# Kernel optimization log

Hardware: AMD Instinct MI355X
Metric: run time of the kernel (lower is better)

Reference implementation:

```python
import jax, jax.numpy as jnp
import numpy as np
from jax import lax

IN_CH = 256
OUT_CH = 256
INTER = IN_CH // 2
KERNEL = 3


def setup_inputs() -> dict:
    key = jax.random.key(0)
    ks = jax.random.split(key, 6)
    B, C, H, W = 8, IN_CH, 128, 128
    x = jax.random.normal(ks[0], (B, C, H, W), dtype=jnp.float32)
    s = 1.0 / np.sqrt(C)
    Wq = jax.random.normal(ks[1], (INTER, C), dtype=jnp.float32) * s
    Wk = jax.random.normal(ks[2], (INTER, C), dtype=jnp.float32) * s
    Wv = jax.random.normal(ks[3], (INTER, C), dtype=jnp.float32) * s
    w1d = jax.random.normal(ks[4], (KERNEL,), dtype=jnp.float32) * (1.0 / np.sqrt(KERNEL))
    Wc = jax.random.normal(ks[5], (OUT_CH, INTER, 3, 3), dtype=jnp.float32) * (1.0 / np.sqrt(INTER * 9))
    return {"x": x, "Wq": Wq, "Wk": Wk, "Wv": Wv, "w1d": w1d, "Wc": Wc}


def reference(x, Wq, Wk, Wv, w1d, Wc):
    B, C, H, W = x.shape
    inter = Wq.shape[0]
    Hs, Ws = H // 4, W // 4  # 1x1 conv, stride 4, pad 0 == spatial subsample
    xs = x[:, :, ::4, ::4]  # [B, C, Hs, Ws]
    q = jnp.einsum('oc,bchw->bohw', Wq, xs).reshape(B, inter, Hs * Ws)  # [B, inter, N]
    k = jnp.einsum('oc,bchw->bohw', Wk, xs).reshape(B, inter, Hs * Ws)
    v = jnp.einsum('oc,bchw->bohw', Wv, xs).reshape(B, inter, Hs * Ws)
    # gate = softmax(Q^T K) over last dim, shape [B, N, N]
    scores = jnp.einsum('bcn,bcm->bnm', q, k)
    gate = jax.nn.softmax(scores, axis=-1)
    # gated value: [B, inter, N] -> [B, inter, Hs, Ws]
    gv = jnp.einsum('bnm,bcm->bcn', gate, v).reshape(B, inter, Hs, Ws)
    # ECA channel gating: global avg pool -> conv1d over channel dim -> sigmoid
    ca = gv.mean(axis=(2, 3))  # [B, inter]
    ca = lax.conv_general_dilated(
        ca[:, None, :],                     # [B, 1, inter]
        w1d[None, None, :],                 # [1, 1, K]
        window_strides=(1,), padding=[((KERNEL - 1) // 2,) * 2],
        dimension_numbers=('NCH', 'OIH', 'NCH'))
    ca = jax.nn.sigmoid(ca)[:, 0, :, None, None]  # [B, inter, 1, 1]
    out = gv * ca
    out = lax.conv_general_dilated(
        out, Wc, window_strides=(1, 1), padding='SAME',
        dimension_numbers=('NCHW', 'OIHW', 'NCHW'))
    return out, gate, ca
```

## Files before the change

### kernel.cpp

```cpp
#include <hip/hip_runtime.h>
#include <math.h>

#define B_   8
#define C_   256
#define CI_  128
#define N_   1024
#define HW_  32
#define CO_  256

typedef __bf16 v8bf __attribute__((ext_vector_type(8)));
typedef float  f32x4 __attribute__((ext_vector_type(4)));
typedef unsigned short ushort_t;

__device__ __forceinline__ unsigned short f2bf_rne(float f) {
    unsigned int u = __float_as_uint(f);
    unsigned int r = u + 0x7FFF + ((u >> 16) & 1);
    return (unsigned short)(r >> 16);
}
__device__ __forceinline__ float bf2f(unsigned short h) {
    return __uint_as_float(((unsigned int)h) << 16);
}
__device__ __forceinline__ v8bf ld8(const ushort_t* p) {
    return *(const v8bf*)p;
}

__global__ __launch_bounds__(256) void prep_all_kernel(
    const float* __restrict__ Wc,
    const float* __restrict__ Wq, const float* __restrict__ Wk,
    const float* __restrict__ Wv,
    ushort_t* __restrict__ Whi, ushort_t* __restrict__ Wlo,
    ushort_t* __restrict__ Wp_hi, ushort_t* __restrict__ Wp_lo,
    float* __restrict__ meanb)
{
    const int bx = blockIdx.x;
    const int tid = threadIdx.x;

    if (bx < 1152) {
        if (bx == 0) {
            *(float4*)&meanb[tid * 4] = make_float4(0.f, 0.f, 0.f, 0.f);
        }
        int idx = bx * 256 + tid;
        int o = idx / 1152;
        int r = idx - o * 1152;
        int ci = r / 9;
        int tap = r - ci * 9;
        float v = Wc[idx];
        unsigned short h = f2bf_rne(v);
        unsigned short l = f2bf_rne(v - bf2f(h));
        int didx = o * 1152 + tap * 128 + ci;
        Whi[didx] = h; Wlo[didx] = l;
    } else {
        int j = (bx - 1152) * 256 + tid;
        int o = j >> 8, c = j & 255;
        float v = (o < 128) ? Wq[o * 256 + c]
                : (o < 256) ? Wk[(o - 128) * 256 + c]
                            : Wv[(o - 256) * 256 + c];
        unsigned short h = f2bf_rne(v);
        unsigned short l = f2bf_rne(v - bf2f(h));
        Wp_hi[j] = h; Wp_lo[j] = l;
    }
}

__global__ __launch_bounds__(256) void proj_fused_kernel(
    const float* __restrict__ x,
    const ushort_t* __restrict__ Wp_hi, const ushort_t* __restrict__ Wp_lo,
    ushort_t* __restrict__ qt_hi, ushort_t* __restrict__ qt_lo,
    ushort_t* __restrict__ kt_hi, ushort_t* __restrict__ kt_lo,
    ushort_t* __restrict__ vB_hi, ushort_t* __restrict__ vB_lo)
{
    __shared__ __align__(16) char xsm[32768];
    const int lin = blockIdx.x;
    const int b  = lin & 7;
    const int n5 = lin >> 3;
    const int n0 = n5 * 32;
    const int tid = threadIdx.x;

    {
        const int w = tid & 31, cg = tid >> 5;
        #pragma unroll
        for (int j = 0; j < 4; ++j) {
            const int cbase = j * 64 + cg * 8;
            float v[8];
            #pragma unroll
            for (int i = 0; i < 8; ++i)
                v[i] = x[((size_t)(b * C_ + cbase + i) * 128 + n5 * 4) * 128 + w * 4];
            unsigned int hw[4], lw[4];
            #pragma unroll
            for (int p = 0; p < 4; ++p) {
                unsigned short h0 = f2bf_rne(v[2 * p]);
                unsigned short l0 = f2bf_rne(v[2 * p] - bf2f(h0));
                unsigned short h1 = f2bf_rne(v[2 * p + 1]);
                unsigned short l1 = f2bf_rne(v[2 * p + 1] - bf2f(h1));
                hw[p] = (unsigned)h0 | ((unsigned)h1 << 16);
                lw[p] = (unsigned)l0 | ((unsigned)l1 << 16);
            }
            const int chunk = j * 8 + cg;
            const int addr = w * 512 + ((chunk ^ (w & 7)) << 4);
            *(uint4*)&xsm[addr]         = make_uint4(hw[0], hw[1], hw[2], hw[3]);
            *(uint4*)&xsm[16384 + addr] = make_uint4(lw[0], lw[1], lw[2], lw[3]);
        }
    }
    __syncthreads();

    const int l = tid & 63, wv = tid >> 6;
    const int ln = l & 15, quad = l >> 4;

    f32x4 acc[6][2];
    #pragma unroll
    for (int t = 0; t < 6; ++t)
        #pragma unroll
        for (int j = 0; j < 2; ++j) acc[t][j] = (f32x4){0.f,0.f,0.f,0.f};

    #pragma unroll 2
    for (int k0 = 0; k0 < 256; k0 += 32) {
        v8bf Bh[2], Bl[2];
        #pragma unroll
        for (int j = 0; j < 2; ++j) {
            int row = j * 16 + ln;
            int chunk = (k0 >> 3) + quad;
            int addr = row * 512 + ((chunk ^ (row & 7)) << 4);
            Bh[j] = *(const v8bf*)&xsm[addr];
            Bl[j] = *(const v8bf*)&xsm[16384 + addr];
        }
        v8bf Ah[6], Al[6];
        #pragma unroll
        for (int t = 0; t < 6; ++t) {
            int st = wv + 4 * t;
            size_t off = (size_t)(st * 16 + ln) * 256 + k0 + quad * 8;
            Ah[t] = ld8(Wp_hi + off); Al[t] = ld8(Wp_lo + off);
        }
        __builtin_amdgcn_s_setprio(1);
        #pragma unroll
        for (int t = 0; t < 4; ++t)
            #pragma unroll
            for (int j = 0; j < 2; ++j) {
                acc[t][j] = __builtin_amdgcn_mfma_f32_16x16x32_bf16(Ah[t], Bh[j], acc[t][j], 0, 0, 0);
                acc[t][j] = __builtin_amdgcn_mfma_f32_16x16x32_bf16(Ah[t], Bl[j], acc[t][j], 0, 0, 0);
                acc[t][j] = __builtin_amdgcn_mfma_f32_16x16x32_bf16(Al[t], Bh[j], acc[t][j], 0, 0, 0);
            }
        #pragma unroll
        for (int t = 4; t < 6; ++t)
            #pragma unroll
            for (int j = 0; j < 2; ++j) {
                acc[t][j] = __builtin_amdgcn_mfma_f32_16x16x32_bf16(Bh[j], Ah[t], acc[t][j], 0, 0, 0);
                acc[t][j] = __builtin_amdgcn_mfma_f32_16x16x32_bf16(Bh[j], Al[t], acc[t][j], 0, 0, 0);
                acc[t][j] = __builtin_amdgcn_mfma_f32_16x16x32_bf16(Bl[j], Ah[t], acc[t][j], 0, 0, 0);
            }
        __builtin_amdgcn_s_setprio(0);
    }

    #pragma unroll
    for (int t = 0; t < 4; ++t) {
        const int st = wv + 4 * t;
        ushort_t* th = (t < 2) ? qt_hi : kt_hi;
        ushort_t* tl = (t < 2) ? qt_lo : kt_lo;
        const int oo = (st & 7) * 16 + quad * 4;
        #pragma unroll
        for (int j = 0; j < 2; ++j) {
            int n = n0 + j * 16 + ln;
            unsigned int h01 = 0, h23 = 0, l01 = 0, l23 = 0;
            #pragma unroll
            for (int r = 0; r < 4; ++r) {
                float f = acc[t][j][r];
                unsigned short hh = f2bf_rne(f);
                unsigned short lo = f2bf_rne(f - bf2f(hh));
                if (r < 2) { h01 |= ((unsigned)hh) << (16 * r); l01 |= ((unsigned)lo) << (16 * r); }
                else       { h23 |= ((unsigned)hh) << (16 * (r - 2)); l23 |= ((unsigned)lo) << (16 * (r - 2)); }
            }
            size_t off = ((size_t)(b * N_) + n) * 128 + oo;
            *(uint2*)&th[off] = make_uint2(h01, h23);
            *(uint2*)&tl[off] = make_uint2(l01, l23);
        }
    }
    #pragma unroll
    for (int t = 4; t < 6; ++t) {
        const int st = wv + 4 * t;
        const int c = (st - 16) * 16 + ln;
        #pragma unroll
        for (int j = 0; j < 2; ++j) {
            int mlo = j * 16 + quad * 4;
            unsigned int h01 = 0, h23 = 0, l01 = 0, l23 = 0;
            #pragma unroll
            for (int r = 0; r < 4; ++r) {
                float f = acc[t][j][r];
                unsigned short hh = f2bf_rne(f);
                unsigned short lo = f2bf_rne(f - bf2f(hh));
                if (r < 2) { h01 |= ((unsigned)hh) << (16 * r); l01 |= ((unsigned)lo) << (16 * r); }
                else       { h23 |= ((unsigned)hh) << (16 * (r - 2)); l23 |= ((unsigned)lo) << (16 * (r - 2)); }
            }
            size_t off = (((size_t)b * 32 + n5) * 128 + c) * 32 + mlo;
            *(uint2*)&vB_hi[off] = make_uint2(h01, h23);
            *(uint2*)&vB_lo[off] = make_uint2(l01, l23);
        }
    }
}

__global__ __launch_bounds__(512, 2) void attn_fused_kernel(
    const ushort_t* __restrict__ qt_hi, const ushort_t* __restrict__ qt_lo,
    const ushort_t* __restrict__ kt_hi, const ushort_t* __restrict__ kt_lo,
    const ushort_t* __restrict__ vB_hi, const ushort_t* __restrict__ vB_lo,
    float* __restrict__ gate, float* __restrict__ gv, float* __restrict__ meanb)
{
    __shared__ __align__(16) char gsm[65536];
    __shared__ float redA[8][32];
    __shared__ float redB[8][32];

    const int lin = blockIdx.x + 32 * blockIdx.y;
    const int b  = lin & 7;
    const int n0 = (lin >> 3) * 32;
    const int tid = threadIdx.x;
    const int l = tid & 63, w = tid >> 6;
    const int ln = l & 15, quad = l >> 4;
    const int Mw = w * 128;

    const ushort_t* qb_h = qt_hi + ((size_t)(b * N_) + n0) * 128;
    const ushort_t* qb_l = qt_lo + ((size_t)(b * N_) + n0) * 128;
    const ushort_t* kb_h = kt_hi + (size_t)(b * N_) * 128;
    const ushort_t* kb_l = kt_lo + (size_t)(b * N_) * 128;

    f32x4 acc[2][8];
    #pragma unroll
    for (int nt = 0; nt < 2; ++nt)
        #pragma unroll
        for (int mt = 0; mt < 8; ++mt) acc[nt][mt] = (f32x4){0.f,0.f,0.f,0.f};

    #pragma unroll
    for (int c0 = 0; c0 < 128; c0 += 32) {
        v8bf Ah[2], Al[2];
        #pragma unroll
        for (int nt = 0; nt < 2; ++nt) {
            size_t aoff = (size_t)(nt * 16 + ln) * 128 + c0 + quad * 8;
            Ah[nt] = ld8(qb_h + aoff); Al[nt] = ld8(qb_l + aoff);
        }
        #pragma unroll
        for (int mt = 0; mt < 8; ++mt) {
            size_t boff = (size_t)(Mw + mt * 16 + ln) * 128 + c0 + quad * 8;
            v8bf Bh = ld8(kb_h + boff);
            v8bf Bl = ld8(kb_l + boff);
            __builtin_amdgcn_s_setprio(1);
            #pragma unroll
            for (int nt = 0; nt < 2; ++nt) {
                acc[nt][mt] = __builtin_amdgcn_mfma_f32_16x16x32_bf16(Ah[nt], Bh, acc[nt][mt], 0, 0, 0);
                acc[nt][mt] = __builtin_amdgcn_mfma_f32_16x16x32_bf16(Ah[nt], Bl, acc[nt][mt], 0, 0, 0);
                acc[nt][mt] = __builtin_amdgcn_mfma_f32_16x16x32_bf16(Al[nt], Bh, acc[nt][mt], 0, 0, 0);
            }
            __builtin_amdgcn_s_setprio(0);
        }
    }

    float rmax[2][4];
    #pragma unroll
    for (int nt = 0; nt < 2; ++nt)
        #pragma unroll
        for (int r = 0; r < 4; ++r) {
            float m = acc[nt][0][r];
            #pragma unroll
            for (int mt = 1; mt < 8; ++mt) m = fmaxf(m, acc[nt][mt][r]);
            rmax[nt][r] = m;
        }
    #pragma unroll
    for (int nt = 0; nt < 2; ++nt)
        #pragma unroll
        for (int r = 0; r < 4; ++r) {
            float m = rmax[nt][r];
            #pragma unroll
            for (int xm = 1; xm <= 8; xm <<= 1) m = fmaxf(m, __shfl_xor(m, xm, 64));
            rmax[nt][r] = m;
        }
    if (ln == 0) {
        #pragma unroll
        for (int nt = 0; nt < 2; ++nt)
            #pragma unroll
            for (int r = 0; r < 4; ++r)
                redA[w][nt * 16 + quad * 4 + r] = rmax[nt][r];
    }
    __syncthreads();
    #pragma unroll
    for (int nt = 0; nt < 2; ++nt)
        #pragma unroll
        for (int r = 0; r < 4; ++r) {
            int row = nt * 16 + quad * 4 + r;
            float m0 = fmaxf(fmaxf(redA[0][row], redA[1][row]),
                             fmaxf(redA[2][row], redA[3][row]));
            float m1 = fmaxf(fmaxf(redA[4][row], redA[5][row]),
                             fmaxf(redA[6][row], redA[7][row]));
            rmax[nt][r] = fmaxf(m0, m1);
        }

    float rsum[2][4];
    #pragma unroll
    for (int nt = 0; nt < 2; ++nt)
        #pragma unroll
        for (int r = 0; r < 4; ++r) {
            float s = 0.f;
            #pragma unroll
            for (int mt = 0; mt < 8; ++mt) {
                float e = __expf(acc[nt][mt][r] - rmax[nt][r]);
                acc[nt][mt][r] = e;
                s += e;
            }
            rsum[nt][r] = s;
        }
    #pragma unroll
    for (int nt = 0; nt < 2; ++nt)
        #pragma unroll
        for (int r = 0; r < 4; ++r) {
            float s = rsum[nt][r];
            #pragma unroll
            for (int xm = 1; xm <= 8; xm <<= 1) s += __shfl_xor(s, xm, 64);
            rsum[nt][r] = s;
        }
    if (ln == 0) {
        #pragma unroll
        for (int nt = 0; nt < 2; ++nt)
            #pragma unroll
            for (int r = 0; r < 4; ++r)
                redB[w][nt * 16 + quad * 4 + r] = rsum[nt][r];
    }
    __syncthreads();
    #pragma unroll
    for (int nt = 0; nt < 2; ++nt)
        #pragma unroll
        for (int r = 0; r < 4; ++r) {
            int row = nt * 16 + quad * 4 + r;
            float inv = 1.0f / ((redB[0][row] + redB[1][row] + redB[2][row] + redB[3][row]) +
                                (redB[4][row] + redB[5][row] + redB[6][row] + redB[7][row]));
            #pragma unroll
            for (int mt = 0; mt < 8; ++mt) acc[nt][mt][r] *= inv;
        }

    #pragma unroll
    for (int nt = 0; nt < 2; ++nt)
        #pragma unroll
        for (int r = 0; r < 4; ++r) {
            int nl = nt * 16 + quad * 4 + r;
            #pragma unroll
            for (int mt = 0; mt < 8; ++mt) {
                int m = Mw + mt * 16 + ln;
                int chunk = m >> 3;
                int addr = nl * 2048 + (((chunk ^ (nl & 7))) << 4) + ((m & 7) << 1);
                *(ushort_t*)&gsm[addr] = f2bf_rne(acc[nt][mt][r]);
            }
        }
    __syncthreads();

    const ushort_t* vb_h = vB_hi + (size_t)b * CI_ * N_;
    const ushort_t* vb_l = vB_lo + (size_t)b * CI_ * N_;

    f32x4 acc2[2];
    acc2[0] = (f32x4){0.f,0.f,0.f,0.f};
    acc2[1] = (f32x4){0.f,0.f,0.f,0.f};

    #pragma unroll 4
    for (int m0 = 0; m0 < 1024; m0 += 32) {
        v8bf Bg[2];
        #pragma unroll
        for (int nt = 0; nt < 2; ++nt) {
            int nl = nt * 16 + ln;
            int chunk = (m0 >> 3) + quad;
            Bg[nt] = *(const v8bf*)&gsm[nl * 2048 + (((chunk ^ (nl & 7))) << 4)];
        }
        int c = w * 16 + ln;
        size_t aoff = (((size_t)(m0 >> 5)) * 128 + c) * 32 + quad * 8;
        v8bf Avh = ld8(vb_h + aoff);
        v8bf Avl = ld8(vb_l + aoff);
        __builtin_amdgcn_s_setprio(1);
        #pragma unroll
        for (int nt = 0; nt < 2; ++nt) {
            acc2[nt] = __builtin_amdgcn_mfma_f32_16x16x32_bf16(Avh, Bg[nt], acc2[nt], 0, 0, 0);
            acc2[nt] = __builtin_amdgcn_mfma_f32_16x16x32_bf16(Avl, Bg[nt], acc2[nt], 0, 0, 0);
        }
        __builtin_amdgcn_s_setprio(0);
    }

    #pragma unroll
    for (int nt = 0; nt < 2; ++nt) {
        int n = n0 + nt * 16 + ln;
        float4 o4 = make_float4(acc2[nt][0], acc2[nt][1], acc2[nt][2], acc2[nt][3]);
        *(float4*)&gv[((size_t)(b * N_) + n) * CI_ + w * 16 + quad * 4] = o4;
    }

    float* grow = gate + (size_t)b * N_ * N_;
    #pragma unroll
    for (int nt = 0; nt < 2; ++nt)
        #pragma unroll
        for (int r = 0; r < 4; ++r) {
            int n = n0 + nt * 16 + quad * 4 + r;
            #pragma unroll
            for (int mt = 0; mt < 8; ++mt) {
                int m = Mw + mt * 16 + ln;
                grow[(size_t)n * N_ + m] = acc[nt][mt][r];
            }
        }

    float s0 = acc2[0][0] + acc2[1][0];
    float s1 = acc2[0][1] + acc2[1][1];
    float s2 = acc2[0][2] + acc2[1][2];
    float s3 = acc2[0][3] + acc2[1][3];
    #pragma unroll
    for (int xm = 1; xm <= 8; xm <<= 1) {
        s0 += __shfl_xor(s0, xm, 64);
        s1 += __shfl_xor(s1, xm, 64);
        s2 += __shfl_xor(s2, xm, 64);
        s3 += __shfl_xor(s3, xm, 64);
    }
    if (ln == 0) {
        int cb = b * CI_ + w * 16 + quad * 4;
        atomicAdd(&meanb[cb + 0], s0);
        atomicAdd(&meanb[cb + 1], s1);
        atomicAdd(&meanb[cb + 2], s2);
        atomicAdd(&meanb[cb + 3], s3);
    }
}

__global__ __launch_bounds__(256) void gvca_prep_kernel(
    const float* __restrict__ gv, const float* __restrict__ meanb,
    const float* __restrict__ w1d,
    ushort_t* __restrict__ gvh, ushort_t* __restrict__ gvl,
    float* __restrict__ ca_out)
{
    __shared__ float ca_s[128];
    const int lin = blockIdx.x;
    const int b  = lin & 7;
    const int ns = lin >> 3;
    const int tid = threadIdx.x;

    if (tid < 128) {
        const float sc = 1.0f / 1024.0f;
        int t = b * 128 + tid;
        float left  = (tid > 0)   ? meanb[t - 1] * sc : 0.0f;
        float mid   = meanb[t] * sc;
        float right = (tid < 127) ? meanb[t + 1] * sc : 0.0f;
        float val = w1d[0] * left + w1d[1] * mid + w1d[2] * right;
        float s = 1.0f / (1.0f + __expf(-val));
        ca_s[tid] = s;
        if (ns == 0) ca_out[t] = s;
    }
    __syncthreads();

    const int cl = (tid & 31) * 4;
    const int nr = tid >> 5;
    #pragma unroll
    for (int i = 0; i < 4; ++i) {
        int n = ns * 32 + nr + i * 8;
        size_t off = ((size_t)(b * N_) + n) * 128 + cl;
        float4 v4 = *(const float4*)&gv[off];
        float vv[4] = { v4.x * ca_s[cl], v4.y * ca_s[cl + 1],
                        v4.z * ca_s[cl + 2], v4.w * ca_s[cl + 3] };
        unsigned int h01 = 0, h23 = 0, l01 = 0, l23 = 0;
        #pragma unroll
        for (int t = 0; t < 4; ++t) {
            unsigned short h = f2bf_rne(vv[t]);
            unsigned short lo = f2bf_rne(vv[t] - bf2f(h));
            if (t < 2) { h01 |= ((unsigned)h) << (16 * t); l01 |= ((unsigned)lo) << (16 * t); }
            else       { h23 |= ((unsigned)h) << (16 * (t - 2)); l23 |= ((unsigned)lo) << (16 * (t - 2)); }
        }
        *(uint2*)&gvh[off] = make_uint2(h01, h23);
        *(uint2*)&gvl[off] = make_uint2(l01, l23);
    }
}

#define CV_BHI  0
#define CV_BLO  26112
__global__ __launch_bounds__(512, 1) void conv_mfma_kernel(
    const ushort_t* __restrict__ gvh, const ushort_t* __restrict__ gvl,
    const ushort_t* __restrict__ Whi, const ushort_t* __restrict__ Wlo,
    float* __restrict__ out)
{
    extern __shared__ __align__(16) char smem[];
    const int AH[2] = {52224, 68608};
    const int AL[2] = {60416, 76800};

    const int lin = blockIdx.x;
    const int b    = lin & 7;
    const int rest = lin >> 3;
    const int o0 = (rest & 3) * 64;
    const int h0 = (rest >> 2) * 4;
    const int tid = threadIdx.x;
    const int l   = tid & 63;
    const int wv  = tid >> 6;
    const int wy  = wv >> 2;
    const int wx  = wv & 3;
    const int ln  = l & 15;
    const int quad = l >> 4;

    f32x4 acc[2][2];
    #pragma unroll
    for (int i = 0; i < 2; ++i)
        #pragma unroll
        for (int j = 0; j < 2; ++j)
            acc[i][j] = (f32x4){0.f, 0.f, 0.f, 0.f};

    const int srow = tid >> 3, scol = tid & 7;
    const int la   = srow * 128 + scol * 16;
    const int csrc = scol ^ (srow & 7);

    for (int half = 0; half < 2; ++half) {
        __syncthreads();
        for (int u = tid; u < 204 * 8; u += 512) {
            int p  = u >> 3;
            int cs = u & 7;
            int hrel = p / 34;
            int c    = p - hrel * 34;
            int gr = h0 + hrel - 1;
            int gc = c - 1;
            bool ok = ((unsigned)gr < 32u) && ((unsigned)gc < 32u);
            uint4 h4 = make_uint4(0, 0, 0, 0), l4 = make_uint4(0, 0, 0, 0);
            if (ok) {
                size_t src = ((size_t)(b * N_) + gr * 32 + gc) * 128 + half * 64 + cs * 8;
                h4 = *(const uint4*)&gvh[src];
                l4 = *(const uint4*)&gvl[src];
            }
            int addr = p * 128 + ((cs ^ (p & 7)) << 4);
            *(uint4*)&smem[CV_BHI + addr] = h4;
            *(uint4*)&smem[CV_BLO + addr] = l4;
        }
        {
            size_t g = (size_t)(o0 + srow) * 1152 + half * 64 + csrc * 8;
            *(uint4*)&smem[AH[0] + la] = *(const uint4*)&Whi[g];
            *(uint4*)&smem[AL[0] + la] = *(const uint4*)&Wlo[g];
        }

        for (int tap = 0; tap < 9; ++tap) {
            __syncthreads();
            uint4 nh, nl;
            if (tap < 8) {
                size_t g = (size_t)(o0 + srow) * 1152 + (tap + 1) * 128 + half * 64 + csrc * 8;
                nh = *(const uint4*)&Whi[g];
                nl = *(const uint4*)&Wlo[g];
            }
            const int ah = AH[tap & 1], al = AL[tap & 1];
            const int dy = tap / 3, dx = tap - dy * 3;
            const int pbase = (wx + dy) * 34 + dx;
            #pragma unroll
            for (int cc = 0; cc < 2; ++cc) {
                v8bf Bh[2], Bl[2], Ah2[2], Al2[2];
                #pragma unroll
                for (int j = 0; j < 2; ++j) {
                    int p = pbase + j * 16 + ln;
                    int ch = cc * 4 + quad;
                    int addr = p * 128 + ((ch ^ (p & 7)) << 4);
                    Bh[j] = *(const v8bf*)&smem[CV_BHI + addr];
                    Bl[j] = *(const v8bf*)&smem[CV_BLO + addr];
                }
                #pragma unroll
                for (int i = 0; i < 2; ++i) {
                    int o = wy * 32 + i * 16 + ln;
                    int ch = cc * 4 + quad;
                    int addr = o * 128 + ((ch ^ (o & 7)) << 4);
                    Ah2[i] = *(const v8bf*)&smem[ah + addr];
                    Al2[i] = *(const v8bf*)&smem[al + addr];
                }
                __builtin_amdgcn_s_setprio(1);
                #pragma unroll
                for (int i = 0; i < 2; ++i)
                    #pragma unroll
                    for (int j = 0; j < 2; ++j) {
                        acc[i][j] = __builtin_amdgcn_mfma_f32_16x16x32_bf16(Ah2[i], Bh[j], acc[i][j], 0, 0, 0);
                        acc[i][j] = __builtin_amdgcn_mfma_f32_16x16x32_bf16(Ah2[i], Bl[j], acc[i][j], 0, 0, 0);
                        acc[i][j] = __builtin_amdgcn_mfma_f32_16x16x32_bf16(Al2[i], Bh[j], acc[i][j], 0, 0, 0);
                    }
                __builtin_amdgcn_s_setprio(0);
            }
            if (tap < 8) {
                int nb = (tap + 1) & 1;
                *(uint4*)&smem[AH[nb] + la] = nh;
                *(uint4*)&smem[AL[nb] + la] = nl;
            }
        }
    }

    const int h = h0 + wx;
    #pragma unroll
    for (int i = 0; i < 2; ++i)
        #pragma unroll
        for (int j = 0; j < 2; ++j)
            #pragma unroll
            for (int r = 0; r < 4; ++r) {
                int o = o0 + wy * 32 + i * 16 + quad * 4 + r;
                int w = j * 16 + ln;
                out[(size_t)(b * CO_ + o) * N_ + h * 32 + w] = acc[i][j][r];
            }
}

extern "C" void kernel_launch(void* const* d_in, const int* in_sizes, int n_in,
                              void* d_out, int out_size, void* d_ws, size_t ws_size,
                              hipStream_t stream) {
    const float* x   = (const float*)d_in[0];
    const float* Wq  = (const float*)d_in[1];
    const float* Wk  = (const float*)d_in[2];
    const float* Wv  = (const float*)d_in[3];
    const float* w1d = (const float*)d_in[4];
    const float* Wc  = (const float*)d_in[5];

    float* out  = (float*)d_out;
    float* gate = out + 2097152;
    float* ca   = gate + 8388608;

    float*    gv      = (float*)d_ws;
    float*    meanb   = gv + 1048576;
    ushort_t* Whi     = (ushort_t*)(meanb + 1024);
    ushort_t* Wlo     = Whi + 294912;
    ushort_t* Wp_hi   = Wlo + 294912;
    ushort_t* Wp_lo   = Wp_hi + 98304;
    ushort_t* qt_hi   = Wp_lo + 98304;
    ushort_t* qt_lo   = qt_hi + 1048576;
    ushort_t* kt_hi   = qt_lo + 1048576;
    ushort_t* kt_lo   = kt_hi + 1048576;
    ushort_t* vB_hi   = kt_lo + 1048576;
    ushort_t* vB_lo   = vB_hi + 1048576;
    ushort_t* gvh     = vB_lo + 1048576;
    ushort_t* gvl     = gvh + 1048576;

    static bool s_attr_done = false;
    if (!s_attr_done) {
        hipFuncSetAttribute((const void*)conv_mfma_kernel,
                            hipFuncAttributeMaxDynamicSharedMemorySize, 84992);
        s_attr_done = true;
    }

    prep_all_kernel<<<dim3(1536), 256, 0, stream>>>(
        Wc, Wq, Wk, Wv, Whi, Wlo, Wp_hi, Wp_lo, meanb);
    proj_fused_kernel<<<dim3(256), 256, 0, stream>>>(
        x, Wp_hi, Wp_lo, qt_hi, qt_lo, kt_hi, kt_lo, vB_hi, vB_lo);
    attn_fused_kernel<<<dim3(32, 8), 512, 0, stream>>>(
        qt_hi, qt_lo, kt_hi, kt_lo, vB_hi, vB_lo, gate, gv, meanb);
    gvca_prep_kernel<<<dim3(256), 256, 0, stream>>>(
        gv, meanb, w1d, gvh, gvl, ca);
    conv_mfma_kernel<<<dim3(256), 512, 84992, stream>>>(
        gvh, gvl, Whi, Wlo, out);
}
```

Measured before the change: 265.1 us.

## Fuse channel-attention gating into attention kernel via cooperative grid sync

Merges the ECA gating/bf16-split pass into the attention kernel. A cooperative launch with a grid-wide barrier waits until all channel-mean atomics have landed, then each block scales its register-resident gv tile and writes the hi/lo bf16 split directly. This removes one kernel launch and the fp32 gv round trip through global memory. In exchange, the grid barrier requires all 256 blocks to be co-resident and adds a global synchronization stall.

```diff
diff --git a/kernel.cpp b/kernel.cpp
--- a/kernel.cpp
+++ b/kernel.cpp
@@ -1,4 +1,5 @@
 #include <hip/hip_runtime.h>
+#include <hip/hip_cooperative_groups.h>
 #include <math.h>
 
 #define B_   8
@@ -199,11 +200,15 @@
     const ushort_t* __restrict__ qt_hi, const ushort_t* __restrict__ qt_lo,
     const ushort_t* __restrict__ kt_hi, const ushort_t* __restrict__ kt_lo,
     const ushort_t* __restrict__ vB_hi, const ushort_t* __restrict__ vB_lo,
-    float* __restrict__ gate, float* __restrict__ gv, float* __restrict__ meanb)
+    float* __restrict__ gate, float* __restrict__ meanb,
+    const float* __restrict__ w1d,
+    ushort_t* __restrict__ gvh, ushort_t* __restrict__ gvl,
+    float* __restrict__ ca_out)
 {
     __shared__ __align__(16) char gsm[65536];
     __shared__ float redA[8][32];
     __shared__ float redB[8][32];
+    __shared__ float ca_s[128];
 
     const int lin = blockIdx.x + 32 * blockIdx.y;
     const int b  = lin & 7;
@@ -373,13 +378,6 @@
         __builtin_amdgcn_s_setprio(0);
     }
 
-    #pragma unroll
-    for (int nt = 0; nt < 2; ++nt) {
-        int n = n0 + nt * 16 + ln;
-        float4 o4 = make_float4(acc2[nt][0], acc2[nt][1], acc2[nt][2], acc2[nt][3]);
-        *(float4*)&gv[((size_t)(b * N_) + n) * CI_ + w * 16 + quad * 4] = o4;
-    }
-
     float* grow = gate + (size_t)b * N_ * N_;
     #pragma unroll
     for (int nt = 0; nt < 2; ++nt)
@@ -411,19 +409,9 @@
         atomicAdd(&meanb[cb + 2], s2);
         atomicAdd(&meanb[cb + 3], s3);
     }
-}
-
-__global__ __launch_bounds__(256) void gvca_prep_kernel(
-    const float* __restrict__ gv, const float* __restrict__ meanb,
-    const float* __restrict__ w1d,
-    ushort_t* __restrict__ gvh, ushort_t* __restrict__ gvl,
-    float* __restrict__ ca_out)
-{
-    __shared__ float ca_s[128];
-    const int lin = blockIdx.x;
-    const int b  = lin & 7;
-    const int ns = lin >> 3;
-    const int tid = threadIdx.x;
+
+    __threadfence();
+    cooperative_groups::this_grid().sync();
 
     if (tid < 128) {
         const float sc = 1.0f / 1024.0f;
@@ -434,27 +422,26 @@
         float val = w1d[0] * left + w1d[1] * mid + w1d[2] * right;
         float s = 1.0f / (1.0f + __expf(-val));
         ca_s[tid] = s;
-        if (ns == 0) ca_out[t] = s;
+        if (n0 == 0) ca_out[t] = s;
     }
     __syncthreads();
 
-    const int cl = (tid & 31) * 4;
-    const int nr = tid >> 5;
-    #pragma unroll
-    for (int i = 0; i < 4; ++i) {
-        int n = ns * 32 + nr + i * 8;
-        size_t off = ((size_t)(b * N_) + n) * 128 + cl;
-        float4 v4 = *(const float4*)&gv[off];
-        float vv[4] = { v4.x * ca_s[cl], v4.y * ca_s[cl + 1],
-                        v4.z * ca_s[cl + 2], v4.w * ca_s[cl + 3] };
+    #pragma unroll
+    for (int nt = 0; nt < 2; ++nt) {
+        int n  = n0 + nt * 16 + ln;
+        int c0 = w * 16 + quad * 4;
+        float vv[4];
+        #pragma unroll
+        for (int r = 0; r < 4; ++r) vv[r] = acc2[nt][r] * ca_s[c0 + r];
         unsigned int h01 = 0, h23 = 0, l01 = 0, l23 = 0;
         #pragma unroll
-        for (int t = 0; t < 4; ++t) {
-            unsigned short h = f2bf_rne(vv[t]);
-            unsigned short lo = f2bf_rne(vv[t] - bf2f(h));
-            if (t < 2) { h01 |= ((unsigned)h) << (16 * t); l01 |= ((unsigned)lo) << (16 * t); }
-            else       { h23 |= ((unsigned)h) << (16 * (t - 2)); l23 |= ((unsigned)lo) << (16 * (t - 2)); }
-        }
+        for (int r = 0; r < 4; ++r) {
+            unsigned short h = f2bf_rne(vv[r]);
+            unsigned short lo = f2bf_rne(vv[r] - bf2f(h));
+            if (r < 2) { h01 |= ((unsigned)h) << (16 * r); l01 |= ((unsigned)lo) << (16 * r); }
+            else       { h23 |= ((unsigned)h) << (16 * (r - 2)); l23 |= ((unsigned)lo) << (16 * (r - 2)); }
+        }
+        size_t off = ((size_t)(b * N_) + n) * 128 + c0;
         *(uint2*)&gvh[off] = make_uint2(h01, h23);
         *(uint2*)&gvl[off] = make_uint2(l01, l23);
     }
@@ -597,8 +584,7 @@
     float* gate = out + 2097152;
     float* ca   = gate + 8388608;
 
-    float*    gv      = (float*)d_ws;
-    float*    meanb   = gv + 1048576;
+    float*    meanb   = (float*)d_ws;
     ushort_t* Whi     = (ushort_t*)(meanb + 1024);
     ushort_t* Wlo     = Whi + 294912;
     ushort_t* Wp_hi   = Wlo + 294912;
@@ -623,10 +609,15 @@
         Wc, Wq, Wk, Wv, Whi, Wlo, Wp_hi, Wp_lo, meanb);
     proj_fused_kernel<<<dim3(256), 256, 0, stream>>>(
         x, Wp_hi, Wp_lo, qt_hi, qt_lo, kt_hi, kt_lo, vB_hi, vB_lo);
-    attn_fused_kernel<<<dim3(32, 8), 512, 0, stream>>>(
-        qt_hi, qt_lo, kt_hi, kt_lo, vB_hi, vB_lo, gate, gv, meanb);
-    gvca_prep_kernel<<<dim3(256), 256, 0, stream>>>(
-        gv, meanb, w1d, gvh, gvl, ca);
+
+    void* attn_args[] = {
+        (void*)&qt_hi, (void*)&qt_lo, (void*)&kt_hi, (void*)&kt_lo,
+        (void*)&vB_hi, (void*)&vB_lo, (void*)&gate, (void*)&meanb,
+        (void*)&w1d, (void*)&gvh, (void*)&gvl, (void*)&ca
+    };
+    hipLaunchCooperativeKernel((void*)attn_fused_kernel, dim3(32, 8), dim3(512),
+                               attn_args, 0, stream);
+
     conv_mfma_kernel<<<dim3(256), 512, 84992, stream>>>(
         gvh, gvl, Whi, Wlo, out);
 }
```

After: 379.4 us. +43.1%, slower.

## Halve attention row tile to 16 rows and stage gate writes through LDS

Applied to the files above, without the earlier changes.

Each attention block now handles 16 query rows instead of 32, which doubles the grid to 512 blocks and halves LDS and accumulator registers so more blocks fit per CU. The gate matrix is no longer written straight from MFMA fragments, which gave scattered 4-byte stores. It is now staged through shared memory in two 8-row passes and written out as coalesced float4 rows. The trade-off is that K and V loads from global memory are repeated across twice as many blocks, and the extra synchronisation passes add overhead.

```diff
diff --git a/kernel.cpp b/kernel.cpp
--- a/kernel.cpp
+++ b/kernel.cpp
@@ -195,19 +195,19 @@
     }
 }
 
-__global__ __launch_bounds__(512, 2) void attn_fused_kernel(
+__global__ __launch_bounds__(512, 4) void attn_fused_kernel(
     const ushort_t* __restrict__ qt_hi, const ushort_t* __restrict__ qt_lo,
     const ushort_t* __restrict__ kt_hi, const ushort_t* __restrict__ kt_lo,
     const ushort_t* __restrict__ vB_hi, const ushort_t* __restrict__ vB_lo,
     float* __restrict__ gate, float* __restrict__ gv, float* __restrict__ meanb)
 {
-    __shared__ __align__(16) char gsm[65536];
-    __shared__ float redA[8][32];
-    __shared__ float redB[8][32];
-
-    const int lin = blockIdx.x + 32 * blockIdx.y;
+    __shared__ __align__(16) char gsm[32768];
+    __shared__ float redA[8][16];
+    __shared__ float redB[8][16];
+
+    const int lin = blockIdx.x;
     const int b  = lin & 7;
-    const int n0 = (lin >> 3) * 32;
+    const int n0 = (lin >> 3) * 16;
     const int tid = threadIdx.x;
     const int l = tid & 63, w = tid >> 6;
     const int ln = l & 15, quad = l >> 4;
@@ -218,198 +218,156 @@
     const ushort_t* kb_h = kt_hi + (size_t)(b * N_) * 128;
     const ushort_t* kb_l = kt_lo + (size_t)(b * N_) * 128;
 
-    f32x4 acc[2][8];
-    #pragma unroll
-    for (int nt = 0; nt < 2; ++nt)
-        #pragma unroll
-        for (int mt = 0; mt < 8; ++mt) acc[nt][mt] = (f32x4){0.f,0.f,0.f,0.f};
+    f32x4 acc[8];
+    #pragma unroll
+    for (int mt = 0; mt < 8; ++mt) acc[mt] = (f32x4){0.f,0.f,0.f,0.f};
 
     #pragma unroll
     for (int c0 = 0; c0 < 128; c0 += 32) {
-        v8bf Ah[2], Al[2];
-        #pragma unroll
-        for (int nt = 0; nt < 2; ++nt) {
-            size_t aoff = (size_t)(nt * 16 + ln) * 128 + c0 + quad * 8;
-            Ah[nt] = ld8(qb_h + aoff); Al[nt] = ld8(qb_l + aoff);
-        }
+        size_t aoff = (size_t)ln * 128 + c0 + quad * 8;
+        v8bf Ah = ld8(qb_h + aoff);
+        v8bf Al = ld8(qb_l + aoff);
         #pragma unroll
         for (int mt = 0; mt < 8; ++mt) {
             size_t boff = (size_t)(Mw + mt * 16 + ln) * 128 + c0 + quad * 8;
             v8bf Bh = ld8(kb_h + boff);
             v8bf Bl = ld8(kb_l + boff);
             __builtin_amdgcn_s_setprio(1);
-            #pragma unroll
-            for (int nt = 0; nt < 2; ++nt) {
-                acc[nt][mt] = __builtin_amdgcn_mfma_f32_16x16x32_bf16(Ah[nt], Bh, acc[nt][mt], 0, 0, 0);
-                acc[nt][mt] = __builtin_amdgcn_mfma_f32_16x16x32_bf16(Ah[nt], Bl, acc[nt][mt], 0, 0, 0);
-                acc[nt][mt] = __builtin_amdgcn_mfma_f32_16x16x32_bf16(Al[nt], Bh, acc[nt][mt], 0, 0, 0);
-            }
+            acc[mt] = __builtin_amdgcn_mfma_f32_16x16x32_bf16(Ah, Bh, acc[mt], 0, 0, 0);
+            acc[mt] = __builtin_amdgcn_mfma_f32_16x16x32_bf16(Ah, Bl, acc[mt], 0, 0, 0);
+            acc[mt] = __builtin_amdgcn_mfma_f32_16x16x32_bf16(Al, Bh, acc[mt], 0, 0, 0);
             __builtin_amdgcn_s_setprio(0);
         }
     }
 
-    float rmax[2][4];
-    #pragma unroll
-    for (int nt = 0; nt < 2; ++nt)
-        #pragma unroll
-        for (int r = 0; r < 4; ++r) {
-            float m = acc[nt][0][r];
-            #pragma unroll
-            for (int mt = 1; mt < 8; ++mt) m = fmaxf(m, acc[nt][mt][r]);
-            rmax[nt][r] = m;
-        }
-    #pragma unroll
-    for (int nt = 0; nt < 2; ++nt)
-        #pragma unroll
-        for (int r = 0; r < 4; ++r) {
-            float m = rmax[nt][r];
-            #pragma unroll
-            for (int xm = 1; xm <= 8; xm <<= 1) m = fmaxf(m, __shfl_xor(m, xm, 64));
-            rmax[nt][r] = m;
-        }
+    float rmax[4];
+    #pragma unroll
+    for (int r = 0; r < 4; ++r) {
+        float m = acc[0][r];
+        #pragma unroll
+        for (int mt = 1; mt < 8; ++mt) m = fmaxf(m, acc[mt][r]);
+        #pragma unroll
+        for (int xm = 1; xm <= 8; xm <<= 1) m = fmaxf(m, __shfl_xor(m, xm, 64));
+        rmax[r] = m;
+    }
     if (ln == 0) {
         #pragma unroll
-        for (int nt = 0; nt < 2; ++nt)
-            #pragma unroll
-            for (int r = 0; r < 4; ++r)
-                redA[w][nt * 16 + quad * 4 + r] = rmax[nt][r];
+        for (int r = 0; r < 4; ++r) redA[w][quad * 4 + r] = rmax[r];
     }
     __syncthreads();
     #pragma unroll
-    for (int nt = 0; nt < 2; ++nt)
-        #pragma unroll
-        for (int r = 0; r < 4; ++r) {
-            int row = nt * 16 + quad * 4 + r;
-            float m0 = fmaxf(fmaxf(redA[0][row], redA[1][row]),
-                             fmaxf(redA[2][row], redA[3][row]));
-            float m1 = fmaxf(fmaxf(redA[4][row], redA[5][row]),
-                             fmaxf(redA[6][row], redA[7][row]));
-            rmax[nt][r] = fmaxf(m0, m1);
-        }
-
-    float rsum[2][4];
-    #pragma unroll
-    for (int nt = 0; nt < 2; ++nt)
-        #pragma unroll
-        for (int r = 0; r < 4; ++r) {
-            float s = 0.f;
-            #pragma unroll
-            for (int mt = 0; mt < 8; ++mt) {
-                float e = __expf(acc[nt][mt][r] - rmax[nt][r]);
-                acc[nt][mt][r] = e;
-                s += e;
-            }
-            rsum[nt][r] = s;
-        }
-    #pragma unroll
-    for (int nt = 0; nt < 2; ++nt)
-        #pragma unroll
-        for (int r = 0; r < 4; ++r) {
-            float s = rsum[nt][r];
-            #pragma unroll
-            for (int xm = 1; xm <= 8; xm <<= 1) s += __shfl_xor(s, xm, 64);
-            rsum[nt][r] = s;
-        }
+    for (int r = 0; r < 4; ++r) {
+        int row = quad * 4 + r;
+        float m0 = fmaxf(fmaxf(redA[0][row], redA[1][row]),
+                         fmaxf(redA[2][row], redA[3][row]));
+        float m1 = fmaxf(fmaxf(redA[4][row], redA[5][row]),
+                         fmaxf(redA[6][row], redA[7][row]));
+        rmax[r] = fmaxf(m0, m1);
+    }
+
+    float rsum[4];
+    #pragma unroll
+    for (int r = 0; r < 4; ++r) {
+        float s = 0.f;
+        #pragma unroll
+        for (int mt = 0; mt < 8; ++mt) {
+            float e = __expf(acc[mt][r] - rmax[r]);
+            acc[mt][r] = e;
+            s += e;
+        }
+        #pragma unroll
+        for (int xm = 1; xm <= 8; xm <<= 1) s += __shfl_xor(s, xm, 64);
+        rsum[r] = s;
+    }
     if (ln == 0) {
         #pragma unroll
-        for (int nt = 0; nt < 2; ++nt)
-            #pragma unroll
-            for (int r = 0; r < 4; ++r)
-                redB[w][nt * 16 + quad * 4 + r] = rsum[nt][r];
+        for (int r = 0; r < 4; ++r) redB[w][quad * 4 + r] = rsum[r];
     }
     __syncthreads();
     #pragma unroll
-    for (int nt = 0; nt < 2; ++nt)
-        #pragma unroll
-        for (int r = 0; r < 4; ++r) {
-            int row = nt * 16 + quad * 4 + r;
-            float inv = 1.0f / ((redB[0][row] + redB[1][row] + redB[2][row] + redB[3][row]) +
-                                (redB[4][row] + redB[5][row] + redB[6][row] + redB[7][row]));
-            #pragma unroll
-            for (int mt = 0; mt < 8; ++mt) acc[nt][mt][r] *= inv;
-        }
-
-    #pragma unroll
-    for (int nt = 0; nt < 2; ++nt)
-        #pragma unroll
-        for (int r = 0; r < 4; ++r) {
-            int nl = nt * 16 + quad * 4 + r;
-            #pragma unroll
-            for (int mt = 0; mt < 8; ++mt) {
-                int m = Mw + mt * 16 + ln;
-                int chunk = m >> 3;
-                int addr = nl * 2048 + (((chunk ^ (nl & 7))) << 4) + ((m & 7) << 1);
-                *(ushort_t*)&gsm[addr] = f2bf_rne(acc[nt][mt][r]);
-            }
-        }
+    for (int r = 0; r < 4; ++r) {
+        int row = quad * 4 + r;
+        float inv = 1.0f / ((redB[0][row] + redB[1][row] + redB[2][row] + redB[3][row]) +
+                            (redB[4][row] + redB[5][row] + redB[6][row] + redB[7][row]));
+        #pragma unroll
+        for (int mt = 0; mt < 8; ++mt) acc[mt][r] *= inv;
+    }
+
+    #pragma unroll
+    for (int r = 0; r < 4; ++r) {
+        int nl = quad * 4 + r;
+        #pragma unroll
+        for (int mt = 0; mt < 8; ++mt) {
+            int m = Mw + mt * 16 + ln;
+            int chunk = m >> 3;
+            int addr = nl * 2048 + (((chunk ^ (nl & 7))) << 4) + ((m & 7) << 1);
+            *(ushort_t*)&gsm[addr] = f2bf_rne(acc[mt][r]);
+        }
+    }
     __syncthreads();
 
     const ushort_t* vb_h = vB_hi + (size_t)b * CI_ * N_;
     const ushort_t* vb_l = vB_lo + (size_t)b * CI_ * N_;
 
-    f32x4 acc2[2];
-    acc2[0] = (f32x4){0.f,0.f,0.f,0.f};
-    acc2[1] = (f32x4){0.f,0.f,0.f,0.f};
+    f32x4 acc2 = (f32x4){0.f,0.f,0.f,0.f};
 
     #pragma unroll 4
     for (int m0 = 0; m0 < 1024; m0 += 32) {
-        v8bf Bg[2];
-        #pragma unroll
-        for (int nt = 0; nt < 2; ++nt) {
-            int nl = nt * 16 + ln;
-            int chunk = (m0 >> 3) + quad;
-            Bg[nt] = *(const v8bf*)&gsm[nl * 2048 + (((chunk ^ (nl & 7))) << 4)];
-        }
+        int chunk = (m0 >> 3) + quad;
+        v8bf Bg = *(const v8bf*)&gsm[ln * 2048 + (((chunk ^ (ln & 7))) << 4)];
         int c = w * 16 + ln;
         size_t aoff = (((size_t)(m0 >> 5)) * 128 + c) * 32 + quad * 8;
         v8bf Avh = ld8(vb_h + aoff);
         v8bf Avl = ld8(vb_l + aoff);
         __builtin_amdgcn_s_setprio(1);
-        #pragma unroll
-        for (int nt = 0; nt < 2; ++nt) {
-            acc2[nt] = __builtin_amdgcn_mfma_f32_16x16x32_bf16(Avh, Bg[nt], acc2[nt], 0, 0, 0);
-            acc2[nt] = __builtin_amdgcn_mfma_f32_16x16x32_bf16(Avl, Bg[nt], acc2[nt], 0, 0, 0);
-        }
+        acc2 = __builtin_amdgcn_mfma_f32_16x16x32_bf16(Avh, Bg, acc2, 0, 0, 0);
+        acc2 = __builtin_amdgcn_mfma_f32_16x16x32_bf16(Avl, Bg, acc2, 0, 0, 0);
         __builtin_amdgcn_s_setprio(0);
     }
 
-    #pragma unroll
-    for (int nt = 0; nt < 2; ++nt) {
-        int n = n0 + nt * 16 + ln;
-        float4 o4 = make_float4(acc2[nt][0], acc2[nt][1], acc2[nt][2], acc2[nt][3]);
+    {
+        int n = n0 + ln;
+        float4 o4 = make_float4(acc2[0], acc2[1], acc2[2], acc2[3]);
         *(float4*)&gv[((size_t)(b * N_) + n) * CI_ + w * 16 + quad * 4] = o4;
     }
 
-    float* grow = gate + (size_t)b * N_ * N_;
-    #pragma unroll
-    for (int nt = 0; nt < 2; ++nt)
-        #pragma unroll
-        for (int r = 0; r < 4; ++r) {
-            int n = n0 + nt * 16 + quad * 4 + r;
-            #pragma unroll
-            for (int mt = 0; mt < 8; ++mt) {
-                int m = Mw + mt * 16 + ln;
-                grow[(size_t)n * N_ + m] = acc[nt][mt][r];
-            }
-        }
-
-    float s0 = acc2[0][0] + acc2[1][0];
-    float s1 = acc2[0][1] + acc2[1][1];
-    float s2 = acc2[0][2] + acc2[1][2];
-    float s3 = acc2[0][3] + acc2[1][3];
-    #pragma unroll
-    for (int xm = 1; xm <= 8; xm <<= 1) {
-        s0 += __shfl_xor(s0, xm, 64);
-        s1 += __shfl_xor(s1, xm, 64);
-        s2 += __shfl_xor(s2, xm, 64);
-        s3 += __shfl_xor(s3, xm, 64);
-    }
-    if (ln == 0) {
-        int cb = b * CI_ + w * 16 + quad * 4;
-        atomicAdd(&meanb[cb + 0], s0);
-        atomicAdd(&meanb[cb + 1], s1);
-        atomicAdd(&meanb[cb + 2], s2);
-        atomicAdd(&meanb[cb + 3], s3);
+    {
+        float s0 = acc2[0], s1 = acc2[1], s2 = acc2[2], s3 = acc2[3];
+        #pragma unroll
+        for (int xm = 1; xm <= 8; xm <<= 1) {
+            s0 += __shfl_xor(s0, xm, 64);
+            s1 += __shfl_xor(s1, xm, 64);
+            s2 += __shfl_xor(s2, xm, 64);
+            s3 += __shfl_xor(s3, xm, 64);
+        }
+        if (ln == 0) {
+            int cb = b * CI_ + w * 16 + quad * 4;
+            atomicAdd(&meanb[cb + 0], s0);
+            atomicAdd(&meanb[cb + 1], s1);
+            atomicAdd(&meanb[cb + 2], s2);
+            atomicAdd(&meanb[cb + 3], s3);
+        }
+    }
+
+    __syncthreads();
+    float* lsm = (float*)gsm;
+    float4* lsm4 = (float4*)gsm;
+    float* grow = gate + (size_t)b * N_ * N_ + (size_t)n0 * N_;
+    #pragma unroll
+    for (int pass = 0; pass < 2; ++pass) {
+        if ((quad >> 1) == pass) {
+            int rowl = (quad & 1) * 4;
+            #pragma unroll
+            for (int r = 0; r < 4; ++r)
+                #pragma unroll
+                for (int mt = 0; mt < 8; ++mt)
+                    lsm[(rowl + r) * 1024 + Mw + mt * 16 + ln] = acc[mt][r];
+        }
+        __syncthreads();
+        float4* g4 = (float4*)(grow + (size_t)pass * 8 * N_);
+        for (int idx = tid; idx < 2048; idx += 512)
+            g4[idx] = lsm4[idx];
+        __syncthreads();
     }
 }
 
@@ -623,7 +581,7 @@
         Wc, Wq, Wk, Wv, Whi, Wlo, Wp_hi, Wp_lo, meanb);
     proj_fused_kernel<<<dim3(256), 256, 0, stream>>>(
         x, Wp_hi, Wp_lo, qt_hi, qt_lo, kt_hi, kt_lo, vB_hi, vB_lo);
-    attn_fused_kernel<<<dim3(32, 8), 512, 0, stream>>>(
+    attn_fused_kernel<<<dim3(512), 512, 0, stream>>>(
         qt_hi, qt_lo, kt_hi, kt_lo, vB_hi, vB_lo, gate, gv, meanb);
     gvca_prep_kernel<<<dim3(256), 256, 0, stream>>>(
         gv, meanb, w1d, gvh, gvl, ca);
```

Measured after the change: 279.0 us. +5.3%, slower.
